# Performance work log

Hardware: AMD Instinct MI355X
Metric: run time of the kernel (lower is better)

## Reference

```python
import jax, jax.numpy as jnp
import numpy as np

B, T, C, H = 4, 2048, 1024, 16


def setup_inputs() -> dict:
    key = jax.random.key(0)
    k1, k2, k3 = jax.random.split(key, 3)
    x = jax.random.normal(k1, (B, T, C), dtype=jnp.float32)
    W_qkv = jax.random.normal(k2, (C, 3 * C), dtype=jnp.float32) * 0.02
    W_proj = jax.random.normal(k3, (C, C), dtype=jnp.float32) * 0.02
    return {"x": x, "W_qkv": W_qkv, "W_proj": W_proj}


def reference(x, W_qkv, W_proj):
    Bc, Tc, Cc = x.shape
    D = Cc // H
    qkv = x @ W_qkv                          # [B,T,3C]
    k, q, v = jnp.split(qkv, 3, axis=-1)     # split order k,q,v as in source
    q = q.reshape(Bc, Tc, H, D)
    k = k.reshape(Bc, Tc, H, D)
    v = v.reshape(Bc, Tc, H, D)
    # NOTE: module scales by full C**-0.5, not head_dim**-0.5
    scale = jnp.asarray(Cc, x.dtype) ** -0.5
    wei = jnp.einsum("bqhd,bkhd->bhqk", q, k) * scale      # [B,H,T,T]
    causal = jnp.tril(jnp.ones((Tc, Tc), dtype=bool))
    wei = jnp.where(causal[None, None], wei, jnp.asarray(-jnp.inf, x.dtype))
    att = jax.nn.softmax(wei, axis=-1)
    out = jnp.einsum("bhqk,bkhd->bqhd", att, v).reshape(Bc, Tc, Cc)
    return out @ W_proj
```

## Files before the change

kernel.cpp:

```cpp
#include <hip/hip_runtime.h>
#include <hip/hip_bf16.h>

#define B_   4
#define T_   2048
#define C_   1024
#define H_   16
#define D_   64
#define NQKV 3072
#define M_   (B_*T_)

typedef __attribute__((ext_vector_type(8))) short bf16x8;
typedef __attribute__((ext_vector_type(4))) short bf16x4;
typedef __attribute__((ext_vector_type(4))) float f32x4;
typedef __hip_bfloat16 bf16;

__device__ inline short f2bs(float f) {
    bf16 h = __float2bfloat16(f);
    return *(short*)&h;
}

__device__ inline float exp2g(float f) { return __builtin_amdgcn_exp2f(f); }

__device__ inline void async_ld16(const bf16* g, const short* l) {
    __builtin_amdgcn_global_load_lds(
        (const __attribute__((address_space(1))) void*)g,
        (__attribute__((address_space(3))) void*)l, 16, 0, 0);
}

__global__ __launch_bounds__(256) void prep(const float* __restrict__ x,
                                            const float* __restrict__ Wqkv,
                                            const float* __restrict__ Wproj,
                                            bf16* __restrict__ xb,
                                            bf16* __restrict__ wqkv_t,
                                            bf16* __restrict__ wproj_t) {
    __shared__ short t[32][33];
    const int bid = blockIdx.x;
    if (bid < 4096) {
        const long i = ((long)bid * 256 + threadIdx.x) * 8;
        const float4 a = *(const float4*)(x + i);
        const float4 bq = *(const float4*)(x + i + 4);
        bf16x8 o;
        o[0] = f2bs(a.x); o[1] = f2bs(a.y); o[2] = f2bs(a.z); o[3] = f2bs(a.w);
        o[4] = f2bs(bq.x); o[5] = f2bs(bq.y); o[6] = f2bs(bq.z); o[7] = f2bs(bq.w);
        *(bf16x8*)(xb + i) = o;
        return;
    }
    const float* in;  bf16* out;  int R, Ccol, r0, c0;
    if (bid < 7168) {
        const int b2 = bid - 4096;
        in = Wqkv; out = wqkv_t; R = C_; Ccol = NQKV;
        c0 = (b2 % 96) * 32; r0 = (b2 / 96) * 32;
    } else {
        const int b3 = bid - 7168;
        in = Wproj; out = wproj_t; R = C_; Ccol = C_;
        c0 = (b3 % 32) * 32; r0 = (b3 / 32) * 32;
    }
    const int xx = threadIdx.x & 31, yy = threadIdx.x >> 5;
#pragma unroll
    for (int i = 0; i < 4; i++)
        t[yy + 8*i][xx] = f2bs(in[(long)(r0 + yy + 8*i) * Ccol + c0 + xx]);
    __syncthreads();
#pragma unroll
    for (int i = 0; i < 4; i++)
        ((short*)out)[(long)(c0 + yy + 8*i) * R + r0 + xx] = t[xx][yy + 8*i];
}

template<int MODE>
__global__ __launch_bounds__(256) void gemm_bt(const bf16* __restrict__ A,
                                               const bf16* __restrict__ Bt,
                                               float* __restrict__ outp,
                                               bf16* __restrict__ qb,
                                               bf16* __restrict__ kb,
                                               bf16* __restrict__ vbT,
                                               int K, int N) {
    __shared__ __align__(16) short SMEM[18432];
    short* As = SMEM;
    short* Bs = SMEM + 8192;
    const int tid  = threadIdx.x;
    const int w    = tid >> 6, lane = tid & 63;
    const int g    = lane >> 4, ln = lane & 15;
    const int m0   = blockIdx.y * 128, n0 = blockIdx.x * 128;
    const int wm   = w & 1, wn = w >> 1;

    f32x4 acc[4][4] = {};

    for (int k0 = 0; k0 < K; k0 += 64) {
#pragma unroll
        for (int i = 0; i < 4; i++) {
            const int s   = w * 256 + i * 64 + lane;
            const int row = s >> 3, c8 = (s & 7) ^ ((s >> 3) & 7);
            async_ld16(A  + (long)(m0 + row) * K + k0 + c8 * 8, &As[s * 8]);
            async_ld16(Bt + (long)(n0 + row) * K + k0 + c8 * 8, &Bs[s * 8]);
        }
        __syncthreads();

#pragma unroll
        for (int kh = 0; kh < 2; kh++) {
            bf16x8 af[4], bfr[4];
#pragma unroll
            for (int i = 0; i < 4; i++)
                af[i]  = *(const bf16x8*)&As[(wm * 64 + i * 16 + ln) * 64 + ((kh * 4 + g) ^ (ln & 7)) * 8];
#pragma unroll
            for (int j = 0; j < 4; j++)
                bfr[j] = *(const bf16x8*)&Bs[(wn * 64 + j * 16 + ln) * 64 + ((kh * 4 + g) ^ (ln & 7)) * 8];
#pragma unroll
            for (int i = 0; i < 4; i++)
#pragma unroll
                for (int j = 0; j < 4; j++)
                    acc[i][j] = __builtin_amdgcn_mfma_f32_16x16x32_bf16(af[i], bfr[j], acc[i][j], 0, 0, 0);
        }
        __syncthreads();
    }

    if (MODE == 0 && n0 >= 2048) {
        short* Vt = SMEM;
#pragma unroll
        for (int i = 0; i < 4; i++)
#pragma unroll
            for (int j = 0; j < 4; j++)
#pragma unroll
                for (int r = 0; r < 4; r++) {
                    const int tl = wm * 64 + i * 16 + g * 4 + r;
                    const int dl = wn * 64 + j * 16 + ln;
                    Vt[dl * 144 + tl] = f2bs(acc[i][j][r]);
                }
        __syncthreads();
        const int b  = m0 >> 11, tb = m0 & (T_ - 1);
        const int h0 = (n0 - 2048) >> 6;
#pragma unroll
        for (int ii = 0; ii < 8; ii++) {
            const int s = ii * 256 + tid;
            const int dl = s >> 4, t16 = s & 15;
            const bf16x8 v = *(const bf16x8*)&Vt[dl * 144 + t16 * 8];
            const int h = h0 + (dl >> 6), d = dl & 63;
            *(bf16x8*)&vbT[(((long)(b * H_ + h)) * D_ + d) * T_ + tb + t16 * 8] = v;
        }
        return;
    }

#pragma unroll
    for (int i = 0; i < 4; i++) {
#pragma unroll
        for (int j = 0; j < 4; j++) {
#pragma unroll
            for (int r = 0; r < 4; r++) {
                const int row = m0 + wm * 64 + i * 16 + g * 4 + r;
                const int col = n0 + wn * 64 + j * 16 + ln;
                if (MODE == 1) {
                    outp[(long)row * N + col] = acc[i][j][r];
                } else {
                    const int b = row >> 11, t = row & (T_ - 1);
                    const int seg = col >> 10;
                    const int c = col & (C_ - 1), h = c >> 6, d = c & 63;
                    if (seg == 0)
                        kb[(((long)(b * H_ + h)) * T_ + t) * D_ + d] = __float2bfloat16(acc[i][j][r]);
                    else
                        qb[(((long)(b * H_ + h)) * T_ + t) * D_ + d] =
                            __float2bfloat16(acc[i][j][r] * (0.03125f * 1.44269504f));
                }
            }
        }
    }
}


__device__ inline void subtile(const bf16x8& qf0, const bf16x8& qf1,
                               f32x4* o, f32x4& l,
                               const short* Ks, const short* Vs, short* myP,
                               int q0, int kbase, int h2, int w, int g, int ln,
                               const bf16x8& ones) {
    f32x4 s[4] = {};
    __builtin_amdgcn_s_setprio(1);
#pragma unroll
    for (int kj = 0; kj < 4; kj++) {
        const int krow = h2 * 64 + kj * 16 + ln;
        const bf16x8 kf0 = *(const bf16x8*)&Ks[krow * 64 + ((0 + g) ^ (krow & 7)) * 8];
        s[kj] = __builtin_amdgcn_mfma_f32_16x16x32_bf16(qf0, kf0, s[kj], 0, 0, 0);
        const bf16x8 kf1 = *(const bf16x8*)&Ks[krow * 64 + ((4 + g) ^ (krow & 7)) * 8];
        s[kj] = __builtin_amdgcn_mfma_f32_16x16x32_bf16(qf1, kf1, s[kj], 0, 0, 0);
    }
    __builtin_amdgcn_s_setprio(0);
    const int rowg = q0 + w * 16 + g * 4;
    if (kbase == q0) {
#pragma unroll
        for (int kj = 0; kj < 4; kj++) {
            const int key = kbase + kj * 16 + ln;
#pragma unroll
            for (int r = 0; r < 4; r++) {
                float p = exp2g(s[kj][r]);
                p = (key <= rowg + r) ? p : 0.f;
                const int prow = g * 4 + r;
                const int pc8 = (kj * 2 + (ln >> 3)) ^ (prow & 7);
                myP[prow * 64 + pc8 * 8 + (ln & 7)] = f2bs(p);
            }
        }
    } else {
#pragma unroll
        for (int kj = 0; kj < 4; kj++) {
#pragma unroll
            for (int r = 0; r < 4; r++) {
                const int prow = g * 4 + r;
                const int pc8 = (kj * 2 + (ln >> 3)) ^ (prow & 7);
                myP[prow * 64 + pc8 * 8 + (ln & 7)] = f2bs(exp2g(s[kj][r]));
            }
        }
    }
    asm volatile("s_waitcnt lgkmcnt(0)" ::: "memory");
    const bf16x8 pf0 = *(const bf16x8*)&myP[ln * 64 + ((0 + g) ^ (ln & 7)) * 8];
    const bf16x8 pf1 = *(const bf16x8*)&myP[ln * 64 + ((4 + g) ^ (ln & 7)) * 8];
    l = __builtin_amdgcn_mfma_f32_16x16x32_bf16(ones, pf0, l, 0, 0, 0);
    l = __builtin_amdgcn_mfma_f32_16x16x32_bf16(ones, pf1, l, 0, 0, 0);
    __builtin_amdgcn_s_setprio(1);
#pragma unroll
    for (int nb = 0; nb < 4; nb++) {
        const int drow = nb * 16 + ln;
        const bf16x8 vf0 = *(const bf16x8*)&Vs[drow * 128 + ((h2 * 8 + 0 + g) ^ (drow & 7)) * 8];
        o[nb] = __builtin_amdgcn_mfma_f32_16x16x32_bf16(vf0, pf0, o[nb], 0, 0, 0);
        const bf16x8 vf1 = *(const bf16x8*)&Vs[drow * 128 + ((h2 * 8 + 4 + g) ^ (drow & 7)) * 8];
        o[nb] = __builtin_amdgcn_mfma_f32_16x16x32_bf16(vf1, pf1, o[nb], 0, 0, 0);
    }
    __builtin_amdgcn_s_setprio(0);
}

__device__ inline void subtile_ab(const bf16x8& qfA0, const bf16x8& qfA1,
                                  const bf16x8& qfB0, const bf16x8& qfB1,
                                  f32x4* oA, f32x4& lA, f32x4* oB, f32x4& lB,
                                  const short* Ks, const short* Vs, short* myP,
                                  int q0A, int kbase, int h2, int w, int g, int ln,
                                  const bf16x8& ones, bool diagA) {
    f32x4 sA[4] = {}, sB[4] = {};
    __builtin_amdgcn_s_setprio(1);
#pragma unroll
    for (int kj = 0; kj < 4; kj++) {
        const int krow = h2 * 64 + kj * 16 + ln;
        const bf16x8 kf0 = *(const bf16x8*)&Ks[krow * 64 + ((0 + g) ^ (krow & 7)) * 8];
        const bf16x8 kf1 = *(const bf16x8*)&Ks[krow * 64 + ((4 + g) ^ (krow & 7)) * 8];
        sA[kj] = __builtin_amdgcn_mfma_f32_16x16x32_bf16(qfA0, kf0, sA[kj], 0, 0, 0);
        sA[kj] = __builtin_amdgcn_mfma_f32_16x16x32_bf16(qfA1, kf1, sA[kj], 0, 0, 0);
        sB[kj] = __builtin_amdgcn_mfma_f32_16x16x32_bf16(qfB0, kf0, sB[kj], 0, 0, 0);
        sB[kj] = __builtin_amdgcn_mfma_f32_16x16x32_bf16(qfB1, kf1, sB[kj], 0, 0, 0);
    }
    __builtin_amdgcn_s_setprio(0);
    const int rowg = q0A + w * 16 + g * 4;
    if (diagA) {
#pragma unroll
        for (int kj = 0; kj < 4; kj++) {
            const int key = kbase + kj * 16 + ln;
#pragma unroll
            for (int r = 0; r < 4; r++) {
                float p = exp2g(sA[kj][r]);
                p = (key <= rowg + r) ? p : 0.f;
                const int prow = g * 4 + r;
                const int pc8 = (kj * 2 + (ln >> 3)) ^ (prow & 7);
                myP[prow * 64 + pc8 * 8 + (ln & 7)] = f2bs(p);
            }
        }
    } else {
#pragma unroll
        for (int kj = 0; kj < 4; kj++)
#pragma unroll
            for (int r = 0; r < 4; r++) {
                const int prow = g * 4 + r;
                const int pc8 = (kj * 2 + (ln >> 3)) ^ (prow & 7);
                myP[prow * 64 + pc8 * 8 + (ln & 7)] = f2bs(exp2g(sA[kj][r]));
            }
    }
    asm volatile("s_waitcnt lgkmcnt(0)" ::: "memory");
    const bf16x8 pfA0 = *(const bf16x8*)&myP[ln * 64 + ((0 + g) ^ (ln & 7)) * 8];
    const bf16x8 pfA1 = *(const bf16x8*)&myP[ln * 64 + ((4 + g) ^ (ln & 7)) * 8];
    lA = __builtin_amdgcn_mfma_f32_16x16x32_bf16(ones, pfA0, lA, 0, 0, 0);
    lA = __builtin_amdgcn_mfma_f32_16x16x32_bf16(ones, pfA1, lA, 0, 0, 0);
#pragma unroll
    for (int kj = 0; kj < 4; kj++)
#pragma unroll
        for (int r = 0; r < 4; r++) {
            const int prow = g * 4 + r;
            const int pc8 = (kj * 2 + (ln >> 3)) ^ (prow & 7);
            myP[prow * 64 + pc8 * 8 + (ln & 7)] = f2bs(exp2g(sB[kj][r]));
        }
    __builtin_amdgcn_s_setprio(1);
#pragma unroll
    for (int nb = 0; nb < 4; nb++) {
        const int drow = nb * 16 + ln;
        const bf16x8 vf0 = *(const bf16x8*)&Vs[drow * 128 + ((h2 * 8 + 0 + g) ^ (drow & 7)) * 8];
        oA[nb] = __builtin_amdgcn_mfma_f32_16x16x32_bf16(vf0, pfA0, oA[nb], 0, 0, 0);
        const bf16x8 vf1 = *(const bf16x8*)&Vs[drow * 128 + ((h2 * 8 + 4 + g) ^ (drow & 7)) * 8];
        oA[nb] = __builtin_amdgcn_mfma_f32_16x16x32_bf16(vf1, pfA1, oA[nb], 0, 0, 0);
    }
    __builtin_amdgcn_s_setprio(0);
    asm volatile("s_waitcnt lgkmcnt(0)" ::: "memory");
    const bf16x8 pfB0 = *(const bf16x8*)&myP[ln * 64 + ((0 + g) ^ (ln & 7)) * 8];
    const bf16x8 pfB1 = *(const bf16x8*)&myP[ln * 64 + ((4 + g) ^ (ln & 7)) * 8];
    lB = __builtin_amdgcn_mfma_f32_16x16x32_bf16(ones, pfB0, lB, 0, 0, 0);
    lB = __builtin_amdgcn_mfma_f32_16x16x32_bf16(ones, pfB1, lB, 0, 0, 0);
    __builtin_amdgcn_s_setprio(1);
#pragma unroll
    for (int nb = 0; nb < 4; nb++) {
        const int drow = nb * 16 + ln;
        const bf16x8 vf0 = *(const bf16x8*)&Vs[drow * 128 + ((h2 * 8 + 0 + g) ^ (drow & 7)) * 8];
        oB[nb] = __builtin_amdgcn_mfma_f32_16x16x32_bf16(vf0, pfB0, oB[nb], 0, 0, 0);
        const bf16x8 vf1 = *(const bf16x8*)&Vs[drow * 128 + ((h2 * 8 + 4 + g) ^ (drow & 7)) * 8];
        oB[nb] = __builtin_amdgcn_mfma_f32_16x16x32_bf16(vf1, pfB1, oB[nb], 0, 0, 0);
    }
    __builtin_amdgcn_s_setprio(0);
}

__device__ inline void stage_kv(const bf16* kbase_p, const bf16* vbase_p,
                                short* KsB, short* VsB, int k0, int tid) {
#pragma unroll
    for (int i = 0; i < 4; i++) {
        const int cc = i * 256 + tid;
        const int key = cc >> 3, kc8 = (cc & 7) ^ (key & 7);
        async_ld16(kbase_p + (long)(k0 + key) * D_ + kc8 * 8, &KsB[cc * 8]);
        const int d = cc >> 4, vc16 = (cc & 15) ^ (d & 7);
        async_ld16(vbase_p + (long)d * T_ + k0 + vc16 * 8, &VsB[cc * 8]);
    }
}

__global__ __launch_bounds__(256, 2) void flash(const bf16* __restrict__ qb,
                                                const bf16* __restrict__ kb,
                                                const bf16* __restrict__ vbT,
                                                bf16* __restrict__ att) {
    __shared__ __align__(16) short Ks[2][128 * 64];
    __shared__ __align__(16) short Vs[2][64 * 128];
    __shared__ __align__(16) short Ps[4 * 16 * 64];
    const int tid = threadIdx.x, w = tid >> 6, lane = tid & 63;
    const int g = lane >> 4, ln = lane & 15;
    const int lin = blockIdx.x;
    const int bh = lin & 63, j = lin >> 6;
    const int b = bh >> 4, h = bh & 15;
    const int q0A = j * 64, q0B = (15 - j) * 64;
    const int q0C = (16 + j) * 64, q0D = (31 - j) * 64;

    const bf16* qpA = qb + ((long)bh * T_ + q0A + w * 16 + ln) * D_;
    const bf16* qpB = qb + ((long)bh * T_ + q0B + w * 16 + ln) * D_;
    const bf16* qpC = qb + ((long)bh * T_ + q0C + w * 16 + ln) * D_;
    const bf16* qpD = qb + ((long)bh * T_ + q0D + w * 16 + ln) * D_;
    const bf16x8 qfA0 = *(const bf16x8*)(qpA + g * 8);
    const bf16x8 qfA1 = *(const bf16x8*)(qpA + 32 + g * 8);
    const bf16x8 qfB0 = *(const bf16x8*)(qpB + g * 8);
    const bf16x8 qfB1 = *(const bf16x8*)(qpB + 32 + g * 8);
    const bf16x8 qfC0 = *(const bf16x8*)(qpC + g * 8);
    const bf16x8 qfC1 = *(const bf16x8*)(qpC + 32 + g * 8);
    const bf16x8 qfD0 = *(const bf16x8*)(qpD + g * 8);
    const bf16x8 qfD1 = *(const bf16x8*)(qpD + 32 + g * 8);

    bf16x8 ones;
#pragma unroll
    for (int i = 0; i < 8; i++) ones[i] = 0x3F80;

    f32x4 oA[4] = {}, oB[4] = {}, oC[4] = {}, oD[4] = {};
    f32x4 lA = {}, lB = {}, lC = {}, lD = {};
    short* myP = &Ps[w * 16 * 64];

    const bf16* kbase_p = kb  + (long)bh * T_ * D_;
    const bf16* vbase_p = vbT + (long)bh * D_ * T_;

    const int nst = (q0D + 64 + 127) >> 7;
    stage_kv(kbase_p, vbase_p, Ks[0], Vs[0], 0, tid);
    __syncthreads();
    for (int s = 0; s < nst; s++) {
        const int k0 = s * 128;
        const int cur = s & 1;
        if (s + 1 < nst)
            stage_kv(kbase_p, vbase_p, Ks[cur ^ 1], Vs[cur ^ 1], k0 + 128, tid);

#pragma unroll
        for (int h2 = 0; h2 < 2; h2++) {
            const int kbase = k0 + h2 * 64;
            if (kbase <= q0A + 63)
                subtile_ab(qfA0, qfA1, qfB0, qfB1, oA, lA, oB, lB,
                           Ks[cur], Vs[cur], myP, q0A, kbase, h2, w, g, ln, ones,
                           kbase == q0A);
            else if (kbase <= q0B + 63)
                subtile(qfB0, qfB1, oB, lB, Ks[cur], Vs[cur], myP, q0B, kbase, h2, w, g, ln, ones);
            if (kbase <= q0C + 63)
                subtile_ab(qfC0, qfC1, qfD0, qfD1, oC, lC, oD, lD,
                           Ks[cur], Vs[cur], myP, q0C, kbase, h2, w, g, ln, ones,
                           kbase == q0C);
            else if (kbase <= q0D + 63)
                subtile(qfD0, qfD1, oD, lD, Ks[cur], Vs[cur], myP, q0D, kbase, h2, w, g, ln, ones);
        }
        __syncthreads();
    }

#pragma unroll
    for (int ti = 0; ti < 4; ti++) {
        const f32x4* o = (ti == 0) ? oA : (ti == 1) ? oB : (ti == 2) ? oC : oD;
        const float lv = (ti == 0) ? lA[0] : (ti == 1) ? lB[0] : (ti == 2) ? lC[0] : lD[0];
        const int q0 = (ti == 0) ? q0A : (ti == 1) ? q0B : (ti == 2) ? q0C : q0D;
        const float invl = 1.f / lv;
        const int q = q0 + w * 16 + ln;
#pragma unroll
        for (int nb = 0; nb < 4; nb++) {
            bf16x4 pk;
#pragma unroll
            for (int r = 0; r < 4; r++) pk[r] = f2bs(o[nb][r] * invl);
            *(bf16x4*)&att[((long)b * T_ + q) * C_ + h * D_ + nb * 16 + g * 4] = pk;
        }
    }
}

extern "C" void kernel_launch(void* const* d_in, const int* in_sizes, int n_in,
                              void* d_out, int out_size, void* d_ws, size_t ws_size,
                              hipStream_t stream) {
    const float* x     = (const float*)d_in[0];
    const float* Wqkv  = (const float*)d_in[1];
    const float* Wproj = (const float*)d_in[2];
    float* out = (float*)d_out;

    char* ws = (char*)d_ws;
    bf16* wqkv_t  = (bf16*)(ws);
    bf16* wproj_t = (bf16*)(ws + 6291456);
    bf16* qb      = (bf16*)(ws + 8388608);
    bf16* kb      = (bf16*)(ws + 25165824);
    bf16* vbT     = (bf16*)(ws + 41943040);
    bf16* xb      = (bf16*)(ws + 58720256);
    bf16* att     = xb;
    (void)ws_size; (void)in_sizes; (void)n_in; (void)out_size;

    prep<<<dim3(8192), dim3(256), 0, stream>>>(x, Wqkv, Wproj, xb, wqkv_t, wproj_t);
    gemm_bt<0><<<dim3(NQKV / 128, M_ / 128), dim3(256), 0, stream>>>(
        xb, wqkv_t, (float*)nullptr, qb, kb, vbT, C_, NQKV);
    flash<<<dim3(512), dim3(256), 0, stream>>>(qb, kb, vbT, att);
    gemm_bt<1><<<dim3(C_ / 128, M_ / 128), dim3(256), 0, stream>>>(
        att, wproj_t, out, (bf16*)nullptr, (bf16*)nullptr, (bf16*)nullptr, C_, C_);
}
```

Before: 238.3 us.

## Process four query tiles per K/V subtile to share K fragment loads

```diff
diff --git a/kernel.cpp b/kernel.cpp
--- a/kernel.cpp
+++ b/kernel.cpp
@@ -164,6 +164,50 @@
 }
 
 
+#define EXPW_P(sx, diag)                                                          \
+    do {                                                                          \
+        if (diag) {                                                               \
+            _Pragma("unroll")                                                     \
+            for (int kj = 0; kj < 4; kj++) {                                      \
+                const int key = kbase + kj * 16 + ln;                             \
+                _Pragma("unroll")                                                 \
+                for (int r = 0; r < 4; r++) {                                     \
+                    float p = exp2g(sx[kj][r]);                                   \
+                    p = (key <= rowg + r) ? p : 0.f;                              \
+                    const int prow = g * 4 + r;                                   \
+                    const int pc8 = (kj * 2 + (ln >> 3)) ^ (prow & 7);            \
+                    myP[prow * 64 + pc8 * 8 + (ln & 7)] = f2bs(p);                \
+                }                                                                 \
+            }                                                                     \
+        } else {                                                                  \
+            _Pragma("unroll")                                                     \
+            for (int kj = 0; kj < 4; kj++)                                        \
+                _Pragma("unroll")                                                 \
+                for (int r = 0; r < 4; r++) {                                     \
+                    const int prow = g * 4 + r;                                   \
+                    const int pc8 = (kj * 2 + (ln >> 3)) ^ (prow & 7);            \
+                    myP[prow * 64 + pc8 * 8 + (ln & 7)] = f2bs(exp2g(sx[kj][r])); \
+                }                                                                 \
+        }                                                                         \
+    } while (0)
+
+#define READ_P(pf0v, pf1v)                                                        \
+    asm volatile("s_waitcnt lgkmcnt(0)" ::: "memory");                            \
+    const bf16x8 pf0v = *(const bf16x8*)&myP[ln * 64 + ((0 + g) ^ (ln & 7)) * 8]; \
+    const bf16x8 pf1v = *(const bf16x8*)&myP[ln * 64 + ((4 + g) ^ (ln & 7)) * 8];
+
+#define PV(ox, pf0v, pf1v)                                                        \
+    __builtin_amdgcn_s_setprio(1);                                                \
+    _Pragma("unroll")                                                             \
+    for (int nb = 0; nb < 4; nb++) {                                              \
+        const int drow = nb * 16 + ln;                                            \
+        const bf16x8 vf0 = *(const bf16x8*)&Vs[drow * 128 + ((h2 * 8 + 0 + g) ^ (drow & 7)) * 8]; \
+        ox[nb] = __builtin_amdgcn_mfma_f32_16x16x32_bf16(vf0, pf0v, ox[nb], 0, 0, 0); \
+        const bf16x8 vf1 = *(const bf16x8*)&Vs[drow * 128 + ((h2 * 8 + 4 + g) ^ (drow & 7)) * 8]; \
+        ox[nb] = __builtin_amdgcn_mfma_f32_16x16x32_bf16(vf1, pf1v, ox[nb], 0, 0, 0); \
+    }                                                                             \
+    __builtin_amdgcn_s_setprio(0);
+
 __device__ inline void subtile(const bf16x8& qf0, const bf16x8& qf1,
                                f32x4* o, f32x4& l,
                                const short* Ks, const short* Vs, short* myP,
@@ -181,45 +225,12 @@
     }
     __builtin_amdgcn_s_setprio(0);
     const int rowg = q0 + w * 16 + g * 4;
-    if (kbase == q0) {
-#pragma unroll
-        for (int kj = 0; kj < 4; kj++) {
-            const int key = kbase + kj * 16 + ln;
-#pragma unroll
-            for (int r = 0; r < 4; r++) {
-                float p = exp2g(s[kj][r]);
-                p = (key <= rowg + r) ? p : 0.f;
-                const int prow = g * 4 + r;
-                const int pc8 = (kj * 2 + (ln >> 3)) ^ (prow & 7);
-                myP[prow * 64 + pc8 * 8 + (ln & 7)] = f2bs(p);
-            }
-        }
-    } else {
-#pragma unroll
-        for (int kj = 0; kj < 4; kj++) {
-#pragma unroll
-            for (int r = 0; r < 4; r++) {
-                const int prow = g * 4 + r;
-                const int pc8 = (kj * 2 + (ln >> 3)) ^ (prow & 7);
-                myP[prow * 64 + pc8 * 8 + (ln & 7)] = f2bs(exp2g(s[kj][r]));
-            }
-        }
-    }
-    asm volatile("s_waitcnt lgkmcnt(0)" ::: "memory");
-    const bf16x8 pf0 = *(const bf16x8*)&myP[ln * 64 + ((0 + g) ^ (ln & 7)) * 8];
-    const bf16x8 pf1 = *(const bf16x8*)&myP[ln * 64 + ((4 + g) ^ (ln & 7)) * 8];
+    const bool diag = (kbase == q0);
+    EXPW_P(s, diag);
+    READ_P(pf0, pf1);
     l = __builtin_amdgcn_mfma_f32_16x16x32_bf16(ones, pf0, l, 0, 0, 0);
     l = __builtin_amdgcn_mfma_f32_16x16x32_bf16(ones, pf1, l, 0, 0, 0);
-    __builtin_amdgcn_s_setprio(1);
-#pragma unroll
-    for (int nb = 0; nb < 4; nb++) {
-        const int drow = nb * 16 + ln;
-        const bf16x8 vf0 = *(const bf16x8*)&Vs[drow * 128 + ((h2 * 8 + 0 + g) ^ (drow & 7)) * 8];
-        o[nb] = __builtin_amdgcn_mfma_f32_16x16x32_bf16(vf0, pf0, o[nb], 0, 0, 0);
-        const bf16x8 vf1 = *(const bf16x8*)&Vs[drow * 128 + ((h2 * 8 + 4 + g) ^ (drow & 7)) * 8];
-        o[nb] = __builtin_amdgcn_mfma_f32_16x16x32_bf16(vf1, pf1, o[nb], 0, 0, 0);
-    }
-    __builtin_amdgcn_s_setprio(0);
+    PV(o, pf0, pf1);
 }
 
 __device__ inline void subtile_ab(const bf16x8& qfA0, const bf16x8& qfA1,
@@ -242,67 +253,65 @@
     }
     __builtin_amdgcn_s_setprio(0);
     const int rowg = q0A + w * 16 + g * 4;
-    if (diagA) {
-#pragma unroll
-        for (int kj = 0; kj < 4; kj++) {
-            const int key = kbase + kj * 16 + ln;
-#pragma unroll
-            for (int r = 0; r < 4; r++) {
-                float p = exp2g(sA[kj][r]);
-                p = (key <= rowg + r) ? p : 0.f;
-                const int prow = g * 4 + r;
-                const int pc8 = (kj * 2 + (ln >> 3)) ^ (prow & 7);
-                myP[prow * 64 + pc8 * 8 + (ln & 7)] = f2bs(p);
-            }
-        }
-    } else {
-#pragma unroll
-        for (int kj = 0; kj < 4; kj++)
-#pragma unroll
-            for (int r = 0; r < 4; r++) {
-                const int prow = g * 4 + r;
-                const int pc8 = (kj * 2 + (ln >> 3)) ^ (prow & 7);
-                myP[prow * 64 + pc8 * 8 + (ln & 7)] = f2bs(exp2g(sA[kj][r]));
-            }
-    }
-    asm volatile("s_waitcnt lgkmcnt(0)" ::: "memory");
-    const bf16x8 pfA0 = *(const bf16x8*)&myP[ln * 64 + ((0 + g) ^ (ln & 7)) * 8];
-    const bf16x8 pfA1 = *(const bf16x8*)&myP[ln * 64 + ((4 + g) ^ (ln & 7)) * 8];
+    EXPW_P(sA, diagA);
+    READ_P(pfA0, pfA1);
     lA = __builtin_amdgcn_mfma_f32_16x16x32_bf16(ones, pfA0, lA, 0, 0, 0);
     lA = __builtin_amdgcn_mfma_f32_16x16x32_bf16(ones, pfA1, lA, 0, 0, 0);
-#pragma unroll
-    for (int kj = 0; kj < 4; kj++)
-#pragma unroll
-        for (int r = 0; r < 4; r++) {
-            const int prow = g * 4 + r;
-            const int pc8 = (kj * 2 + (ln >> 3)) ^ (prow & 7);
-            myP[prow * 64 + pc8 * 8 + (ln & 7)] = f2bs(exp2g(sB[kj][r]));
-        }
-    __builtin_amdgcn_s_setprio(1);
-#pragma unroll
-    for (int nb = 0; nb < 4; nb++) {
-        const int drow = nb * 16 + ln;
-        const bf16x8 vf0 = *(const bf16x8*)&Vs[drow * 128 + ((h2 * 8 + 0 + g) ^ (drow & 7)) * 8];
-        oA[nb] = __builtin_amdgcn_mfma_f32_16x16x32_bf16(vf0, pfA0, oA[nb], 0, 0, 0);
-        const bf16x8 vf1 = *(const bf16x8*)&Vs[drow * 128 + ((h2 * 8 + 4 + g) ^ (drow & 7)) * 8];
-        oA[nb] = __builtin_amdgcn_mfma_f32_16x16x32_bf16(vf1, pfA1, oA[nb], 0, 0, 0);
-    }
-    __builtin_amdgcn_s_setprio(0);
-    asm volatile("s_waitcnt lgkmcnt(0)" ::: "memory");
-    const bf16x8 pfB0 = *(const bf16x8*)&myP[ln * 64 + ((0 + g) ^ (ln & 7)) * 8];
-    const bf16x8 pfB1 = *(const bf16x8*)&myP[ln * 64 + ((4 + g) ^ (ln & 7)) * 8];
+    EXPW_P(sB, false);
+    PV(oA, pfA0, pfA1);
+    READ_P(pfB0, pfB1);
     lB = __builtin_amdgcn_mfma_f32_16x16x32_bf16(ones, pfB0, lB, 0, 0, 0);
     lB = __builtin_amdgcn_mfma_f32_16x16x32_bf16(ones, pfB1, lB, 0, 0, 0);
+    PV(oB, pfB0, pfB1);
+}
+
+__device__ inline void subtile_quad(const bf16x8& qfA0, const bf16x8& qfA1,
+                                    const bf16x8& qfB0, const bf16x8& qfB1,
+                                    const bf16x8& qfC0, const bf16x8& qfC1,
+                                    const bf16x8& qfD0, const bf16x8& qfD1,
+                                    f32x4* oA, f32x4& lA, f32x4* oB, f32x4& lB,
+                                    f32x4* oC, f32x4& lC, f32x4* oD, f32x4& lD,
+                                    const short* Ks, const short* Vs, short* myP,
+                                    int q0A, int kbase, int h2, int w, int g, int ln,
+                                    const bf16x8& ones, bool diagA) {
+    f32x4 sA[4] = {}, sB[4] = {}, sC[4] = {}, sD[4] = {};
     __builtin_amdgcn_s_setprio(1);
 #pragma unroll
-    for (int nb = 0; nb < 4; nb++) {
-        const int drow = nb * 16 + ln;
-        const bf16x8 vf0 = *(const bf16x8*)&Vs[drow * 128 + ((h2 * 8 + 0 + g) ^ (drow & 7)) * 8];
-        oB[nb] = __builtin_amdgcn_mfma_f32_16x16x32_bf16(vf0, pfB0, oB[nb], 0, 0, 0);
-        const bf16x8 vf1 = *(const bf16x8*)&Vs[drow * 128 + ((h2 * 8 + 4 + g) ^ (drow & 7)) * 8];
-        oB[nb] = __builtin_amdgcn_mfma_f32_16x16x32_bf16(vf1, pfB1, oB[nb], 0, 0, 0);
+    for (int kj = 0; kj < 4; kj++) {
+        const int krow = h2 * 64 + kj * 16 + ln;
+        const bf16x8 kf0 = *(const bf16x8*)&Ks[krow * 64 + ((0 + g) ^ (krow & 7)) * 8];
+        const bf16x8 kf1 = *(const bf16x8*)&Ks[krow * 64 + ((4 + g) ^ (krow & 7)) * 8];
+        sA[kj] = __builtin_amdgcn_mfma_f32_16x16x32_bf16(qfA0, kf0, sA[kj], 0, 0, 0);
+        sA[kj] = __builtin_amdgcn_mfma_f32_16x16x32_bf16(qfA1, kf1, sA[kj], 0, 0, 0);
+        sB[kj] = __builtin_amdgcn_mfma_f32_16x16x32_bf16(qfB0, kf0, sB[kj], 0, 0, 0);
+        sB[kj] = __builtin_amdgcn_mfma_f32_16x16x32_bf16(qfB1, kf1, sB[kj], 0, 0, 0);
+        sC[kj] = __builtin_amdgcn_mfma_f32_16x16x32_bf16(qfC0, kf0, sC[kj], 0, 0, 0);
+        sC[kj] = __builtin_amdgcn_mfma_f32_16x16x32_bf16(qfC1, kf1, sC[kj], 0, 0, 0);
+        sD[kj] = __builtin_amdgcn_mfma_f32_16x16x32_bf16(qfD0, kf0, sD[kj], 0, 0, 0);
+        sD[kj] = __builtin_amdgcn_mfma_f32_16x16x32_bf16(qfD1, kf1, sD[kj], 0, 0, 0);
     }
     __builtin_amdgcn_s_setprio(0);
+    const int rowg = q0A + w * 16 + g * 4;
+    EXPW_P(sA, diagA);
+    READ_P(pfA0, pfA1);
+    lA = __builtin_amdgcn_mfma_f32_16x16x32_bf16(ones, pfA0, lA, 0, 0, 0);
+    lA = __builtin_amdgcn_mfma_f32_16x16x32_bf16(ones, pfA1, lA, 0, 0, 0);
+    EXPW_P(sB, false);
+    PV(oA, pfA0, pfA1);
+    READ_P(pfB0, pfB1);
+    lB = __builtin_amdgcn_mfma_f32_16x16x32_bf16(ones, pfB0, lB, 0, 0, 0);
+    lB = __builtin_amdgcn_mfma_f32_16x16x32_bf16(ones, pfB1, lB, 0, 0, 0);
+    EXPW_P(sC, false);
+    PV(oB, pfB0, pfB1);
+    READ_P(pfC0, pfC1);
+    lC = __builtin_amdgcn_mfma_f32_16x16x32_bf16(ones, pfC0, lC, 0, 0, 0);
+    lC = __builtin_amdgcn_mfma_f32_16x16x32_bf16(ones, pfC1, lC, 0, 0, 0);
+    EXPW_P(sD, false);
+    PV(oC, pfC0, pfC1);
+    READ_P(pfD0, pfD1);
+    lD = __builtin_amdgcn_mfma_f32_16x16x32_bf16(ones, pfD0, lD, 0, 0, 0);
+    lD = __builtin_amdgcn_mfma_f32_16x16x32_bf16(ones, pfD1, lD, 0, 0, 0);
+    PV(oD, pfD0, pfD1);
 }
 
 __device__ inline void stage_kv(const bf16* kbase_p, const bf16* vbase_p,
@@ -368,18 +377,23 @@
 #pragma unroll
         for (int h2 = 0; h2 < 2; h2++) {
             const int kbase = k0 + h2 * 64;
-            if (kbase <= q0A + 63)
-                subtile_ab(qfA0, qfA1, qfB0, qfB1, oA, lA, oB, lB,
-                           Ks[cur], Vs[cur], myP, q0A, kbase, h2, w, g, ln, ones,
-                           kbase == q0A);
-            else if (kbase <= q0B + 63)
-                subtile(qfB0, qfB1, oB, lB, Ks[cur], Vs[cur], myP, q0B, kbase, h2, w, g, ln, ones);
-            if (kbase <= q0C + 63)
+            if (kbase <= q0A + 63) {
+                subtile_quad(qfA0, qfA1, qfB0, qfB1, qfC0, qfC1, qfD0, qfD1,
+                             oA, lA, oB, lB, oC, lC, oD, lD,
+                             Ks[cur], Vs[cur], myP, q0A, kbase, h2, w, g, ln, ones,
+                             kbase == q0A);
+            } else if (kbase <= q0B + 63) {
+                subtile_ab(qfB0, qfB1, qfC0, qfC1, oB, lB, oC, lC,
+                           Ks[cur], Vs[cur], myP, q0B, kbase, h2, w, g, ln, ones,
+                           kbase == q0B);
+                subtile(qfD0, qfD1, oD, lD, Ks[cur], Vs[cur], myP, q0D, kbase, h2, w, g, ln, ones);
+            } else if (kbase <= q0C + 63) {
                 subtile_ab(qfC0, qfC1, qfD0, qfD1, oC, lC, oD, lD,
                            Ks[cur], Vs[cur], myP, q0C, kbase, h2, w, g, ln, ones,
                            kbase == q0C);
-            else if (kbase <= q0D + 63)
+            } else if (kbase <= q0D + 63) {
                 subtile(qfD0, qfD1, oD, lD, Ks[cur], Vs[cur], myP, q0D, kbase, h2, w, g, ln, ones);
+            }
         }
         __syncthreads();
     }
```

New measurement: 250.0 us. 4.9% more time.
